# Performance work log

Hardware: AMD Instinct MI355X
Metric: run time of the kernel (lower is better)

The kernel has to match this reference:

```python
import jax, jax.numpy as jnp
import numpy as np

D_MODEL = 512
N_HEADS = 8
D_K = 64
N_GENE = 16384
N_TF = 512


def setup_inputs() -> dict:
    key = jax.random.key(0)
    ks = jax.random.split(key, 12)
    HD = N_HEADS * D_K
    s = 1.0 / np.sqrt(D_MODEL)
    inp = {
        "H_TF": jax.random.normal(ks[0], (N_TF, D_MODEL), jnp.float32),
        "H_G": jax.random.normal(ks[1], (N_GENE, D_MODEL), jnp.float32),
        "z_exp": jax.random.normal(ks[2], (N_GENE, D_MODEL), jnp.float32),
        "z_seq": jax.random.normal(ks[3], (N_GENE, D_MODEL), jnp.float32),
        "z_txt": jax.random.normal(ks[4], (N_GENE, D_MODEL), jnp.float32),
        "tf_idx": jax.random.randint(ks[5], (N_TF,), 0, N_GENE, jnp.int64)
        if jax.config.jax_enable_x64 else jax.random.randint(ks[5], (N_TF,), 0, N_GENE, jnp.int32),
        "Wq_seq": jax.random.normal(ks[6], (D_MODEL, HD), jnp.float32) * s,
        "Wk_seq": jax.random.normal(ks[7], (D_MODEL, HD), jnp.float32) * s,
        "Wq_exp": jax.random.normal(ks[8], (D_MODEL, HD), jnp.float32) * s,
        "Wk_exp": jax.random.normal(ks[9], (D_MODEL, HD), jnp.float32) * s,
        "Wq_txt": jax.random.normal(ks[10], (D_MODEL, HD), jnp.float32) * s,
        "Wk_txt": jax.random.normal(ks[11], (D_MODEL, HD), jnp.float32) * s,
        # gate initialized as identity per head, zero bias (as in nn.init.eye_)
        "gate_weight": jnp.tile(jnp.eye(3, dtype=jnp.float32)[None], (N_HEADS, 1, 1)),
        "gate_bias": jnp.zeros((N_HEADS, 3), jnp.float32),
    }
    return inp


def reference(H_TF, H_G, z_exp, z_seq, z_txt, tf_idx,
              Wq_seq, Wk_seq, Wq_exp, Wk_exp, Wq_txt, Wk_txt,
              gate_weight, gate_bias):
    n_tf, n_gene = H_TF.shape[0], H_G.shape[0]
    H, dk = N_HEADS, D_K
    scale = jnp.sqrt(jnp.asarray(dk, H_TF.dtype))

    def qk_score(z, Wq, Wk):
        Q = (z[tf_idx] @ Wq).reshape(n_tf, H, dk)   # [t,h,d]
        K = (z @ Wk).reshape(n_gene, H, dk)          # [g,h,d]
        return jnp.einsum('thd,ghd->htg', Q, K) / scale  # [h,t,g]

    s_bind = qk_score(z_seq, Wq_seq, Wk_seq)
    s_coexpr = qk_score(z_exp, Wq_exp, Wk_exp)
    s_know = qk_score(z_txt, Wq_txt, Wk_txt)

    # evidence gate: per-head 3x3 mixing + softmax over evidence axis
    s = jnp.stack([s_bind, s_coexpr, s_know], axis=-1)        # [h,t,g,3]
    gate_logits = jnp.einsum('htge,hef->htgf', s, gate_weight) + gate_bias[:, None, None, :]
    alpha = jax.nn.softmax(gate_logits, axis=-1)               # [h,t,g,3]

    u = alpha[..., 0] * s_bind + alpha[..., 1] * s_coexpr + alpha[..., 2] * s_know
    A = jax.nn.softmax(u, axis=-1)                             # softmax over genes

    u_mean = u.mean(axis=0)          # [t,g]
    A_mean = A.mean(axis=0)          # [t,g]
    alpha_mean = alpha.mean(axis=0)  # [t,g,3]
    return (H_TF, H_G, A_mean, u_mean, alpha_mean)
```

## Files before the change

kernel.cpp:

```cpp
#include <hip/hip_runtime.h>
#include <hip/hip_bf16.h>
#include <stdint.h>

typedef __attribute__((ext_vector_type(4))) float f32x4;
typedef __attribute__((ext_vector_type(8))) short bf16x8;

#define N_GENE 16384
#define N_TF   512
#define DMODEL 512
#define L2E    1.44269504088896340736f

__device__ __forceinline__ float bf2f(unsigned short u) {
    union { unsigned int i; float f; } v; v.i = ((unsigned int)u) << 16; return v.f;
}
__device__ __forceinline__ unsigned short f2bf(float f) {
    unsigned int r;
    asm("v_cvt_pk_bf16_f32 %0, %1, %1" : "=v"(r) : "v"(f));
    return (unsigned short)r;
}
__device__ __forceinline__ float fast_rcp(float x) {
    float r; asm("v_rcp_f32 %0, %1" : "=v"(r) : "v"(x)); return r;
}
__device__ __forceinline__ float fast_exp2(float x) {
    float r; asm("v_exp_f32 %0, %1" : "=v"(r) : "v"(x)); return r;
}

#define GLOBAL_AS(p) ((const __attribute__((address_space(1))) void*)(p))
#define LDS_AS(p)    ((__attribute__((address_space(3))) void*)(p))

__global__ void zerof(float* __restrict__ p, int n) {
    int i = blockIdx.x * blockDim.x + threadIdx.x;
    if (i < n) p[i] = 0.f;
}

__global__ void copy16(const int4* __restrict__ src, int4* __restrict__ dst, int n) {
    int i = blockIdx.x * blockDim.x + threadIdx.x;
    if (i < n) dst[i] = src[i];
}

__global__ __launch_bounds__(256) void cvt3(const float* __restrict__ z0, const float* __restrict__ z1,
                                            const float* __restrict__ z2, unsigned short* __restrict__ dst) {
    const float* s = blockIdx.z == 0 ? z0 : (blockIdx.z == 1 ? z1 : z2);
    size_t i = ((size_t)blockIdx.x * 256 + threadIdx.x) * 8;
    float4 a = *(const float4*)(s + i);
    float4 b = *(const float4*)(s + i + 4);
    unsigned int w0, w1, w2, w3;
    asm("v_cvt_pk_bf16_f32 %0, %1, %2" : "=v"(w0) : "v"(a.x), "v"(a.y));
    asm("v_cvt_pk_bf16_f32 %0, %1, %2" : "=v"(w1) : "v"(a.z), "v"(a.w));
    asm("v_cvt_pk_bf16_f32 %0, %1, %2" : "=v"(w2) : "v"(b.x), "v"(b.y));
    asm("v_cvt_pk_bf16_f32 %0, %1, %2" : "=v"(w3) : "v"(b.z), "v"(b.w));
    uint4 o; o.x = w0; o.y = w1; o.z = w2; o.w = w3;
    *(uint4*)(dst + (size_t)blockIdx.z * (size_t)N_GENE * 512 + i) = o;
}

__global__ void transpose6(const float* __restrict__ s0, const float* __restrict__ s1,
                           const float* __restrict__ s2, const float* __restrict__ s3,
                           const float* __restrict__ s4, const float* __restrict__ s5,
                           unsigned short* __restrict__ dst) {
    const float* srcs[6] = { s0, s1, s2, s3, s4, s5 };
    int m = blockIdx.z;
    __shared__ unsigned short tile[32][33];
    int x = blockIdx.x * 32 + threadIdx.x;
    int y0 = blockIdx.y * 32;
    const float* src = srcs[m];
    for (int i = threadIdx.y; i < 32; i += 8)
        tile[i][threadIdx.x] = f2bf(src[(size_t)(y0 + i) * 512 + x]);
    __syncthreads();
    int xo = blockIdx.y * 32 + threadIdx.x;
    int yo0 = blockIdx.x * 32;
    unsigned short* d = dst + (size_t)m * 512 * 512;
    for (int i = threadIdx.y; i < 32; i += 8)
        d[(size_t)(yo0 + i) * 512 + xo] = tile[threadIdx.x][i];
}

__global__ __launch_bounds__(256) void gemm_bf16(const unsigned short* __restrict__ A,
                                                 const unsigned short* __restrict__ Bt,
                                                 unsigned short* __restrict__ C,
                                                 const int* __restrict__ idx) {
    __shared__ unsigned short As[128 * 64];
    __shared__ unsigned short Bs[128 * 64];
    const int tid = threadIdx.x;
    const int lane = tid & 63;
    const int w = tid >> 6;
    const int mBase = blockIdx.y * 128;
    const int nBase = blockIdx.x * 128;
    const int wm = (w & 1) * 64;
    const int wn = (w >> 1) * 64;
    const int lm = lane & 15, lq = lane >> 4;

    const int rbase = tid >> 3;
    const int seg = tid & 7;
    const int scol = ((seg ^ (rbase & 7)) << 3);
    const unsigned short* aSrc[4];
    const unsigned short* bSrc[4];
    #pragma unroll
    for (int i = 0; i < 4; ++i) {
        int r = i * 32 + rbase;
        int ar = idx ? idx[mBase + r] : (mBase + r);
        aSrc[i] = A + (size_t)ar * 512 + scol;
        bSrc[i] = Bt + (size_t)(nBase + r) * 512 + scol;
    }
    const int ldsOfs = (tid & 192) * 8;

    f32x4 acc[4][4] = {};

    for (int k0 = 0; k0 < 512; k0 += 64) {
        #pragma unroll
        for (int i = 0; i < 4; ++i) {
            __builtin_amdgcn_global_load_lds(GLOBAL_AS(aSrc[i] + k0), LDS_AS(As + i * 2048 + ldsOfs), 16, 0, 0);
            __builtin_amdgcn_global_load_lds(GLOBAL_AS(bSrc[i] + k0), LDS_AS(Bs + i * 2048 + ldsOfs), 16, 0, 0);
        }
        __syncthreads();
        bf16x8 af[4][2], bfr[4][2];
        #pragma unroll
        for (int mt = 0; mt < 4; ++mt) {
            int row = wm + mt * 16 + lm;
            int sw = row & 7;
            #pragma unroll
            for (int hh = 0; hh < 2; ++hh)
                af[mt][hh] = *(const bf16x8*)(As + row * 64 + (((hh * 4 + lq) ^ sw) << 3));
        }
        #pragma unroll
        for (int nt = 0; nt < 4; ++nt) {
            int row = wn + nt * 16 + lm;
            int sw = row & 7;
            #pragma unroll
            for (int hh = 0; hh < 2; ++hh)
                bfr[nt][hh] = *(const bf16x8*)(Bs + row * 64 + (((hh * 4 + lq) ^ sw) << 3));
        }
        #pragma unroll
        for (int mt = 0; mt < 4; ++mt)
            #pragma unroll
            for (int nt = 0; nt < 4; ++nt) {
                acc[mt][nt] = __builtin_amdgcn_mfma_f32_16x16x32_bf16(af[mt][0], bfr[nt][0], acc[mt][nt], 0, 0, 0);
                acc[mt][nt] = __builtin_amdgcn_mfma_f32_16x16x32_bf16(af[mt][1], bfr[nt][1], acc[mt][nt], 0, 0, 0);
            }
        __syncthreads();
    }
    #pragma unroll
    for (int mt = 0; mt < 4; ++mt)
        #pragma unroll
        for (int nt = 0; nt < 4; ++nt)
            #pragma unroll
            for (int r = 0; r < 4; ++r) {
                int m = mBase + wm + mt * 16 + lq * 4 + r;
                int n = nBase + wn + nt * 16 + lm;
                C[(size_t)m * 512 + n] = f2bf(acc[mt][nt][r]);
            }
}

__global__ __launch_bounds__(256, 4) void score_pass(const unsigned short* __restrict__ Qp,
                                                     const unsigned short* __restrict__ Kp,
                                                     const float* __restrict__ gw,
                                                     const float* __restrict__ gb,
                                                     unsigned short* __restrict__ p_out,
                                                     float* __restrict__ l_out,
                                                     float* __restrict__ u_mean,
                                                     float* __restrict__ alpha_mean)
{
    const int tid = threadIdx.x;
    const int lane = tid & 63;
    const int w = tid >> 6;
    const int tw = blockIdx.y * 128 + w * 32;
    const int g0 = blockIdx.x * 32;
    const int lm = lane & 15, lq = lane >> 4;

    float u_sum[2][2][4] = {};
    float a0_sum[2][2][4] = {};
    float a1_sum[2][2][4] = {};

    #pragma unroll 1
    for (int h = 0; h < 8; ++h) {
        float W2[3][3], B2[3];
        #pragma unroll
        for (int e = 0; e < 3; ++e)
            #pragma unroll
            for (int f = 0; f < 3; ++f) W2[e][f] = gw[(h * 3 + e) * 3 + f] * (0.125f * L2E);
        #pragma unroll
        for (int f = 0; f < 3; ++f) B2[f] = gb[h * 3 + f] * L2E;

        f32x4 s[3][2][2];
        #pragma unroll
        for (int e = 0; e < 3; ++e) {
            const unsigned short* qbase = Qp + (size_t)e * 512 * 512 + (size_t)(tw + lm) * 512 + h * 64 + lq * 8;
            const unsigned short* kbase = Kp + (size_t)e * N_GENE * 512 + (size_t)(g0 + lm) * 512 + h * 64 + lq * 8;
            bf16x8 q[2][2], k[2][2];
            #pragma unroll
            for (int mt = 0; mt < 2; ++mt) {
                q[mt][0] = *(const bf16x8*)(qbase + mt * 16 * 512);
                q[mt][1] = *(const bf16x8*)(qbase + mt * 16 * 512 + 32);
            }
            #pragma unroll
            for (int nt = 0; nt < 2; ++nt) {
                k[nt][0] = *(const bf16x8*)(kbase + nt * 16 * 512);
                k[nt][1] = *(const bf16x8*)(kbase + nt * 16 * 512 + 32);
            }
            #pragma unroll
            for (int mt = 0; mt < 2; ++mt)
                #pragma unroll
                for (int nt = 0; nt < 2; ++nt) {
                    f32x4 a = {};
                    a = __builtin_amdgcn_mfma_f32_16x16x32_bf16(q[mt][0], k[nt][0], a, 0, 0, 0);
                    a = __builtin_amdgcn_mfma_f32_16x16x32_bf16(q[mt][1], k[nt][1], a, 0, 0, 0);
                    s[e][mt][nt] = a;
                }
        }
        float lpart[2][4] = {};
        #pragma unroll
        for (int mt = 0; mt < 2; ++mt)
            #pragma unroll
            for (int nt = 0; nt < 2; ++nt) {
                unsigned short* pb = p_out + ((size_t)h * N_TF + (tw + mt * 16 + lq * 4)) * N_GENE + (g0 + nt * 16 + lm);
                #pragma unroll
                for (int r = 0; r < 4; ++r) {
                    float s0 = s[0][mt][nt][r];
                    float s1 = s[1][mt][nt][r];
                    float s2 = s[2][mt][nt][r];
                    float gl0 = fmaf(s2, W2[2][0], fmaf(s1, W2[1][0], fmaf(s0, W2[0][0], B2[0])));
                    float gl1 = fmaf(s2, W2[2][1], fmaf(s1, W2[1][1], fmaf(s0, W2[0][1], B2[1])));
                    float gl2 = fmaf(s2, W2[2][2], fmaf(s1, W2[1][2], fmaf(s0, W2[0][2], B2[2])));
                    float e0 = fast_exp2(gl0), e1 = fast_exp2(gl1), e2 = fast_exp2(gl2);
                    float rz = fast_rcp(e0 + e1 + e2);
                    float a0 = e0 * rz, a1 = e1 * rz;
                    float dot = fmaf(e0, s0, fmaf(e1, s1, e2 * s2));
                    float u = dot * (rz * 0.125f);
                    float pv = fast_exp2(u * L2E);
                    u_sum[mt][nt][r] += u;
                    a0_sum[mt][nt][r] += a0;
                    a1_sum[mt][nt][r] += a1;
                    lpart[mt][r] += pv;
                    pb[(size_t)r * N_GENE] = f2bf(pv);
                }
            }
        #pragma unroll
        for (int mt = 0; mt < 2; ++mt)
            #pragma unroll
            for (int r = 0; r < 4; ++r) {
                float v = lpart[mt][r];
                v += __shfl_xor(v, 1);
                v += __shfl_xor(v, 2);
                v += __shfl_xor(v, 4);
                v += __shfl_xor(v, 8);
                if (lm == 0) atomicAdd(&l_out[h * N_TF + tw + mt * 16 + lq * 4 + r], v);
            }
    }
    #pragma unroll
    for (int mt = 0; mt < 2; ++mt)
        #pragma unroll
        for (int nt = 0; nt < 2; ++nt)
            #pragma unroll
            for (int r = 0; r < 4; ++r) {
                int t = tw + mt * 16 + lq * 4 + r;
                int g = g0 + nt * 16 + lm;
                u_mean[(size_t)t * N_GENE + g] = u_sum[mt][nt][r] * 0.125f;
                float a0m = a0_sum[mt][nt][r] * 0.125f;
                float a1m = a1_sum[mt][nt][r] * 0.125f;
                size_t base = ((size_t)t * N_GENE + g) * 3;
                alpha_mean[base + 0] = a0m;
                alpha_mean[base + 1] = a1m;
                alpha_mean[base + 2] = 1.0f - a0m - a1m;
            }
}

__global__ __launch_bounds__(256) void finalize_A(const unsigned short* __restrict__ p,
                                                  const float* __restrict__ l,
                                                  float* __restrict__ A_mean) {
    const int t = blockIdx.x;
    float rinv[8];
    #pragma unroll
    for (int h = 0; h < 8; ++h) rinv[h] = 0.125f / l[h * N_TF + t];
    for (int g4 = threadIdx.x * 4; g4 < N_GENE; g4 += 256 * 4) {
        float s0 = 0.f, s1 = 0.f, s2 = 0.f, s3 = 0.f;
        #pragma unroll
        for (int h = 0; h < 8; ++h) {
            ushort4 pv = *(const ushort4*)(p + ((size_t)h * N_TF + t) * N_GENE + g4);
            float r = rinv[h];
            s0 += bf2f(pv.x) * r; s1 += bf2f(pv.y) * r; s2 += bf2f(pv.z) * r; s3 += bf2f(pv.w) * r;
        }
        float4 o; o.x = s0; o.y = s1; o.z = s2; o.w = s3;
        *(float4*)(A_mean + (size_t)t * N_GENE + g4) = o;
    }
}

extern "C" void kernel_launch(void* const* d_in, const int* in_sizes, int n_in,
                              void* d_out, int out_size, void* d_ws, size_t ws_size,
                              hipStream_t stream) {
    const float* H_TF  = (const float*)d_in[0];
    const float* H_G   = (const float*)d_in[1];
    const float* z[3]  = { (const float*)d_in[3], (const float*)d_in[2], (const float*)d_in[4] };
    const int* tf_idx  = (const int*)d_in[5];
    const float* Wq[3] = { (const float*)d_in[6], (const float*)d_in[8], (const float*)d_in[10] };
    const float* Wk[3] = { (const float*)d_in[7], (const float*)d_in[9], (const float*)d_in[11] };
    const float* gw    = (const float*)d_in[12];
    const float* gb    = (const float*)d_in[13];
    float* out = (float*)d_out;

    float* out_HTF   = out;
    float* out_HG    = out + 262144;
    float* out_Amean = out + 262144 + 8388608;
    float* out_umean = out + 262144 + 8388608 + 8388608;
    float* out_alpha = out + 262144 + 8388608 + 8388608 + 8388608;

    unsigned short* Wt = (unsigned short*)d_ws;
    unsigned short* Kp = Wt + 6 * 262144;
    unsigned short* Qp = Kp + 3 * (size_t)N_GENE * 512;
    unsigned short* Pp = Qp + 3 * 512 * 512;
    float*          Lp = (float*)(Pp + (size_t)8 * N_TF * N_GENE);
    unsigned short* Zb = Pp;

    zerof<<<16, 256, 0, stream>>>(Lp, 8 * N_TF);

    transpose6<<<dim3(16, 16, 6), dim3(32, 8), 0, stream>>>(
        Wq[0], Wk[0], Wq[1], Wk[1], Wq[2], Wk[2], Wt);

    cvt3<<<dim3(N_GENE * 512 / (256 * 8), 1, 3), 256, 0, stream>>>(z[0], z[1], z[2], Zb);

    for (int e = 0; e < 3; ++e) {
        const unsigned short* zb = Zb + (size_t)e * N_GENE * 512;
        gemm_bf16<<<dim3(4, 128), 256, 0, stream>>>(zb, Wt + (size_t)(e * 2 + 1) * 262144,
                                                    Kp + (size_t)e * N_GENE * 512, nullptr);
        gemm_bf16<<<dim3(4, 4), 256, 0, stream>>>(zb, Wt + (size_t)(e * 2) * 262144,
                                                  Qp + (size_t)e * 512 * 512, tf_idx);
    }

    score_pass<<<dim3(N_GENE / 32, N_TF / 128), 256, 0, stream>>>(
        Qp, Kp, gw, gb, Pp, Lp, out_umean, out_alpha);

    finalize_A<<<N_TF, 256, 0, stream>>>(Pp, Lp, out_Amean);

    copy16<<<(262144 * 4 / 16 + 255) / 256, 256, 0, stream>>>((const int4*)H_TF, (int4*)out_HTF, 262144 * 4 / 16);
    copy16<<<(8388608 * 4 / 16 + 255) / 256, 256, 0, stream>>>((const int4*)H_G, (int4*)out_HG, 8388608 * 4 / 16);
}
```

Before: 786.9 us.

## Merge launches, retile score pass, add nontemporal stores and wider finalize loads

```diff
diff --git a/kernel.cpp b/kernel.cpp
--- a/kernel.cpp
+++ b/kernel.cpp
@@ -4,6 +4,7 @@
 
 typedef __attribute__((ext_vector_type(4))) float f32x4;
 typedef __attribute__((ext_vector_type(8))) short bf16x8;
+typedef __attribute__((ext_vector_type(8))) unsigned short u16x8;
 
 #define N_GENE 16384
 #define N_TF   512
@@ -28,61 +29,79 @@
 #define GLOBAL_AS(p) ((const __attribute__((address_space(1))) void*)(p))
 #define LDS_AS(p)    ((__attribute__((address_space(3))) void*)(p))
 
-__global__ void zerof(float* __restrict__ p, int n) {
-    int i = blockIdx.x * blockDim.x + threadIdx.x;
-    if (i < n) p[i] = 0.f;
-}
-
-__global__ void copy16(const int4* __restrict__ src, int4* __restrict__ dst, int n) {
-    int i = blockIdx.x * blockDim.x + threadIdx.x;
-    if (i < n) dst[i] = src[i];
-}
-
-__global__ __launch_bounds__(256) void cvt3(const float* __restrict__ z0, const float* __restrict__ z1,
-                                            const float* __restrict__ z2, unsigned short* __restrict__ dst) {
-    const float* s = blockIdx.z == 0 ? z0 : (blockIdx.z == 1 ? z1 : z2);
-    size_t i = ((size_t)blockIdx.x * 256 + threadIdx.x) * 8;
-    float4 a = *(const float4*)(s + i);
-    float4 b = *(const float4*)(s + i + 4);
-    unsigned int w0, w1, w2, w3;
-    asm("v_cvt_pk_bf16_f32 %0, %1, %2" : "=v"(w0) : "v"(a.x), "v"(a.y));
-    asm("v_cvt_pk_bf16_f32 %0, %1, %2" : "=v"(w1) : "v"(a.z), "v"(a.w));
-    asm("v_cvt_pk_bf16_f32 %0, %1, %2" : "=v"(w2) : "v"(b.x), "v"(b.y));
-    asm("v_cvt_pk_bf16_f32 %0, %1, %2" : "=v"(w3) : "v"(b.z), "v"(b.w));
-    uint4 o; o.x = w0; o.y = w1; o.z = w2; o.w = w3;
-    *(uint4*)(dst + (size_t)blockIdx.z * (size_t)N_GENE * 512 + i) = o;
-}
-
-__global__ void transpose6(const float* __restrict__ s0, const float* __restrict__ s1,
-                           const float* __restrict__ s2, const float* __restrict__ s3,
-                           const float* __restrict__ s4, const float* __restrict__ s5,
-                           unsigned short* __restrict__ dst) {
-    const float* srcs[6] = { s0, s1, s2, s3, s4, s5 };
-    int m = blockIdx.z;
+__global__ __launch_bounds__(256) void prep(const float* __restrict__ z0, const float* __restrict__ z1,
+                                            const float* __restrict__ z2, unsigned short* __restrict__ zb,
+                                            const float* __restrict__ w0, const float* __restrict__ w1,
+                                            const float* __restrict__ w2, const float* __restrict__ w3,
+                                            const float* __restrict__ w4, const float* __restrict__ w5,
+                                            unsigned short* __restrict__ wt, float* __restrict__ lp) {
     __shared__ unsigned short tile[32][33];
-    int x = blockIdx.x * 32 + threadIdx.x;
-    int y0 = blockIdx.y * 32;
-    const float* src = srcs[m];
-    for (int i = threadIdx.y; i < 32; i += 8)
-        tile[i][threadIdx.x] = f2bf(src[(size_t)(y0 + i) * 512 + x]);
-    __syncthreads();
-    int xo = blockIdx.y * 32 + threadIdx.x;
-    int yo0 = blockIdx.x * 32;
-    unsigned short* d = dst + (size_t)m * 512 * 512;
-    for (int i = threadIdx.y; i < 32; i += 8)
-        d[(size_t)(yo0 + i) * 512 + xo] = tile[threadIdx.x][i];
-}
-
-__global__ __launch_bounds__(256) void gemm_bf16(const unsigned short* __restrict__ A,
-                                                 const unsigned short* __restrict__ Bt,
-                                                 unsigned short* __restrict__ C,
-                                                 const int* __restrict__ idx) {
+    const int b = blockIdx.x;
+    const int tid = threadIdx.x;
+    if (b < 12288) {
+        const float* s = b < 4096 ? z0 : (b < 8192 ? z1 : z2);
+        const int m = b >> 12;
+        const int blk = b & 4095;
+        size_t i = ((size_t)blk * 256 + tid) * 8;
+        float4 a = *(const float4*)(s + i);
+        float4 c = *(const float4*)(s + i + 4);
+        unsigned int q0, q1, q2, q3;
+        asm("v_cvt_pk_bf16_f32 %0, %1, %2" : "=v"(q0) : "v"(a.x), "v"(a.y));
+        asm("v_cvt_pk_bf16_f32 %0, %1, %2" : "=v"(q1) : "v"(a.z), "v"(a.w));
+        asm("v_cvt_pk_bf16_f32 %0, %1, %2" : "=v"(q2) : "v"(c.x), "v"(c.y));
+        asm("v_cvt_pk_bf16_f32 %0, %1, %2" : "=v"(q3) : "v"(c.z), "v"(c.w));
+        uint4 o; o.x = q0; o.y = q1; o.z = q2; o.w = q3;
+        *(uint4*)(zb + (size_t)m * (size_t)N_GENE * 512 + i) = o;
+    } else if (b < 13824) {
+        const float* srcs[6] = { w0, w1, w2, w3, w4, w5 };
+        const int b2 = b - 12288;
+        const int m = b2 >> 8;
+        const int rem = b2 & 255;
+        const int by = rem >> 4, bx = rem & 15;
+        const int tx = tid & 31, ty8 = tid >> 5;
+        const float* src = srcs[m];
+        const int x = bx * 32 + tx;
+        const int y0 = by * 32;
+        for (int i = ty8; i < 32; i += 8)
+            tile[i][tx] = f2bf(src[(size_t)(y0 + i) * 512 + x]);
+        __syncthreads();
+        const int xo = by * 32 + tx;
+        const int yo0 = bx * 32;
+        unsigned short* d = wt + (size_t)m * 512 * 512;
+        for (int i = ty8; i < 32; i += 8)
+            d[(size_t)(yo0 + i) * 512 + xo] = tile[tx][i];
+    } else {
+        for (int i = tid; i < 8 * N_TF; i += 256) lp[i] = 0.f;
+    }
+}
+
+__global__ __launch_bounds__(256) void gemm_all(const unsigned short* __restrict__ Zb,
+                                                const unsigned short* __restrict__ Wt,
+                                                unsigned short* __restrict__ Kp,
+                                                unsigned short* __restrict__ Qp,
+                                                const int* __restrict__ tf_idx) {
     __shared__ unsigned short As[128 * 64];
     __shared__ unsigned short Bs[128 * 64];
+    const int e = blockIdx.z;
+    const unsigned short* A = Zb + (size_t)e * N_GENE * 512;
+    const unsigned short* Bt;
+    unsigned short* C;
+    const int* idx;
+    int mBase;
+    if (blockIdx.y < 128) {
+        Bt = Wt + (size_t)(e * 2 + 1) * 262144;
+        C = Kp + (size_t)e * N_GENE * 512;
+        idx = nullptr;
+        mBase = blockIdx.y * 128;
+    } else {
+        Bt = Wt + (size_t)(e * 2) * 262144;
+        C = Qp + (size_t)e * 512 * 512;
+        idx = tf_idx;
+        mBase = (blockIdx.y - 128) * 128;
+    }
     const int tid = threadIdx.x;
     const int lane = tid & 63;
     const int w = tid >> 6;
-    const int mBase = blockIdx.y * 128;
     const int nBase = blockIdx.x * 128;
     const int wm = (w & 1) * 64;
     const int wn = (w >> 1) * 64;
@@ -161,8 +180,12 @@
     const int tid = threadIdx.x;
     const int lane = tid & 63;
     const int w = tid >> 6;
-    const int tw = blockIdx.y * 128 + w * 32;
-    const int g0 = blockIdx.x * 32;
+    const int bid = blockIdx.x;
+    const int o = (bid & 7) * 256 + (bid >> 3);
+    const int gx = o >> 3;
+    const int ty = o & 7;
+    const int tw = ty * 64 + (w & 1) * 32;
+    const int g0 = gx * 64 + (w >> 1) * 32;
     const int lm = lane & 15, lq = lane >> 4;
 
     float u_sum[2][2][4] = {};
@@ -229,7 +252,7 @@
                     a0_sum[mt][nt][r] += a0;
                     a1_sum[mt][nt][r] += a1;
                     lpart[mt][r] += pv;
-                    pb[(size_t)r * N_GENE] = f2bf(pv);
+                    __builtin_nontemporal_store(f2bf(pv), pb + (size_t)r * N_GENE);
                 }
             }
         #pragma unroll
@@ -252,13 +275,13 @@
             for (int r = 0; r < 4; ++r) {
                 int t = tw + mt * 16 + lq * 4 + r;
                 int g = g0 + nt * 16 + lm;
-                u_mean[(size_t)t * N_GENE + g] = u_sum[mt][nt][r] * 0.125f;
+                __builtin_nontemporal_store(u_sum[mt][nt][r] * 0.125f, u_mean + (size_t)t * N_GENE + g);
                 float a0m = a0_sum[mt][nt][r] * 0.125f;
                 float a1m = a1_sum[mt][nt][r] * 0.125f;
                 size_t base = ((size_t)t * N_GENE + g) * 3;
-                alpha_mean[base + 0] = a0m;
-                alpha_mean[base + 1] = a1m;
-                alpha_mean[base + 2] = 1.0f - a0m - a1m;
+                __builtin_nontemporal_store(a0m, alpha_mean + base + 0);
+                __builtin_nontemporal_store(a1m, alpha_mean + base + 1);
+                __builtin_nontemporal_store(1.0f - a0m - a1m, alpha_mean + base + 2);
             }
 }
 
@@ -269,16 +292,35 @@
     float rinv[8];
     #pragma unroll
     for (int h = 0; h < 8; ++h) rinv[h] = 0.125f / l[h * N_TF + t];
-    for (int g4 = threadIdx.x * 4; g4 < N_GENE; g4 += 256 * 4) {
-        float s0 = 0.f, s1 = 0.f, s2 = 0.f, s3 = 0.f;
+    const int gbase = blockIdx.y * 4096 + threadIdx.x * 8;
+    #pragma unroll
+    for (int gg = 0; gg < 2; ++gg) {
+        int g8 = gbase + gg * 2048;
+        float s[8] = {};
         #pragma unroll
         for (int h = 0; h < 8; ++h) {
-            ushort4 pv = *(const ushort4*)(p + ((size_t)h * N_TF + t) * N_GENE + g4);
+            u16x8 pv = __builtin_nontemporal_load((const u16x8*)(p + ((size_t)h * N_TF + t) * N_GENE + g8));
             float r = rinv[h];
-            s0 += bf2f(pv.x) * r; s1 += bf2f(pv.y) * r; s2 += bf2f(pv.z) * r; s3 += bf2f(pv.w) * r;
-        }
-        float4 o; o.x = s0; o.y = s1; o.z = s2; o.w = s3;
-        *(float4*)(A_mean + (size_t)t * N_GENE + g4) = o;
+            #pragma unroll
+            for (int j = 0; j < 8; ++j) s[j] += bf2f(pv[j]) * r;
+        }
+        f32x4 o0, o1;
+        o0[0] = s[0]; o0[1] = s[1]; o0[2] = s[2]; o0[3] = s[3];
+        o1[0] = s[4]; o1[1] = s[5]; o1[2] = s[6]; o1[3] = s[7];
+        __builtin_nontemporal_store(o0, (f32x4*)(A_mean + (size_t)t * N_GENE + g8));
+        __builtin_nontemporal_store(o1, (f32x4*)(A_mean + (size_t)t * N_GENE + g8 + 4));
+    }
+}
+
+__global__ __launch_bounds__(256) void copy_all(const int4* __restrict__ a, const int4* __restrict__ b,
+                                                int4* __restrict__ da, int4* __restrict__ db) {
+    const int bx = blockIdx.x;
+    if (bx < 256) {
+        int i = bx * 256 + threadIdx.x;
+        da[i] = a[i];
+    } else {
+        int i = (bx - 256) * 256 + threadIdx.x;
+        db[i] = b[i];
     }
 }
 
@@ -308,26 +350,15 @@
     float*          Lp = (float*)(Pp + (size_t)8 * N_TF * N_GENE);
     unsigned short* Zb = Pp;
 
-    zerof<<<16, 256, 0, stream>>>(Lp, 8 * N_TF);
-
-    transpose6<<<dim3(16, 16, 6), dim3(32, 8), 0, stream>>>(
-        Wq[0], Wk[0], Wq[1], Wk[1], Wq[2], Wk[2], Wt);
-
-    cvt3<<<dim3(N_GENE * 512 / (256 * 8), 1, 3), 256, 0, stream>>>(z[0], z[1], z[2], Zb);
-
-    for (int e = 0; e < 3; ++e) {
-        const unsigned short* zb = Zb + (size_t)e * N_GENE * 512;
-        gemm_bf16<<<dim3(4, 128), 256, 0, stream>>>(zb, Wt + (size_t)(e * 2 + 1) * 262144,
-                                                    Kp + (size_t)e * N_GENE * 512, nullptr);
-        gemm_bf16<<<dim3(4, 4), 256, 0, stream>>>(zb, Wt + (size_t)(e * 2) * 262144,
-                                                  Qp + (size_t)e * 512 * 512, tf_idx);
-    }
-
-    score_pass<<<dim3(N_GENE / 32, N_TF / 128), 256, 0, stream>>>(
-        Qp, Kp, gw, gb, Pp, Lp, out_umean, out_alpha);
-
-    finalize_A<<<N_TF, 256, 0, stream>>>(Pp, Lp, out_Amean);
-
-    copy16<<<(262144 * 4 / 16 + 255) / 256, 256, 0, stream>>>((const int4*)H_TF, (int4*)out_HTF, 262144 * 4 / 16);
-    copy16<<<(8388608 * 4 / 16 + 255) / 256, 256, 0, stream>>>((const int4*)H_G, (int4*)out_HG, 8388608 * 4 / 16);
-}
+    prep<<<13825, 256, 0, stream>>>(z[0], z[1], z[2], Zb,
+                                    Wq[0], Wk[0], Wq[1], Wk[1], Wq[2], Wk[2], Wt, Lp);
+
+    gemm_all<<<dim3(4, 132, 3), 256, 0, stream>>>(Zb, Wt, Kp, Qp, tf_idx);
+
+    score_pass<<<2048, 256, 0, stream>>>(Qp, Kp, gw, gb, Pp, Lp, out_umean, out_alpha);
+
+    finalize_A<<<dim3(512, 4), 256, 0, stream>>>(Pp, Lp, out_Amean);
+
+    copy_all<<<256 + 8192, 256, 0, stream>>>((const int4*)H_TF, (const int4*)H_G,
+                                             (int4*)out_HTF, (int4*)out_HG);
+}
```

Result: faster. 674.4 us (-14.3%).
